# Kernel optimization log

Measured on AMD Instinct MI355X. Metric: run time of the kernel, lower is better.

Reference implementation:

```python
import jax, jax.numpy as jnp
import numpy as np

B, S, D, H = 4, 2048, 512, 8  # batch, seq, input_dim=feature_dim, n_heads


def setup_inputs() -> dict:
    key = jax.random.key(0)
    ks = jax.random.split(key, 12)
    s = 1.0 / np.sqrt(D)
    return {
        "q": jax.random.normal(ks[0], (B, S, D), jnp.float32),
        "k": jax.random.normal(ks[1], (B, S, D), jnp.float32),
        "v": jax.random.normal(ks[2], (B, S, D), jnp.float32),
        "mask": jax.random.randint(ks[3], (B, S), 0, 2, jnp.int32),
        "wq": jax.random.uniform(ks[4], (D, D), jnp.float32, -s, s),
        "bq": jax.random.uniform(ks[5], (D,), jnp.float32, -s, s),
        "wk": jax.random.uniform(ks[6], (D, D), jnp.float32, -s, s),
        "bk": jax.random.uniform(ks[7], (D,), jnp.float32, -s, s),
        "wv": jax.random.uniform(ks[8], (D, D), jnp.float32, -s, s),
        "bv": jax.random.uniform(ks[9], (D,), jnp.float32, -s, s),
        "wd": jax.random.uniform(ks[10], (D, D), jnp.float32, -s, s),
        "bd": jax.random.uniform(ks[11], (D,), jnp.float32, -s, s),
    }


def reference(q, k, v, mask, wq, bq, wk, bk, wv, bv, wd, bd):
    hd = D // H
    # linear projections [B,S,D]
    qp = q @ wq + bq
    kp = k @ wk + bk
    vp = v @ wv + bv
    # split heads -> [B,H,S,hd]
    split = lambda x: x.reshape(B, S, H, hd).transpose(0, 2, 1, 3)
    qh, kh, vh = split(qp), split(kp), split(vp)
    # scaled dot-product attention with additive mask [B,1,1,S]
    scores = jnp.einsum("bhqd,bhkd->bhqk", qh, kh) / np.sqrt(hd)
    scores = scores + mask.astype(scores.dtype)[:, None, None, :] * (-1e9)
    weights = jax.nn.softmax(scores, axis=-1)
    attn = jnp.einsum("bhqk,bhkd->bhqd", weights, vh)
    # merge heads -> [B,S,D], final dense
    attn = attn.transpose(0, 2, 1, 3).reshape(B, S, D)
    return attn @ wd + bd
```

## Files before the change

kernel.cpp:

```cpp
#include <hip/hip_runtime.h>
#include <hip/hip_bf16.h>
#include <cmath>

typedef __bf16 bf16;
typedef __attribute__((ext_vector_type(8))) __bf16 bf16x8;
typedef __attribute__((ext_vector_type(4))) __bf16 bf16x4;
typedef __attribute__((ext_vector_type(4))) float f32x4;
typedef __attribute__((ext_vector_type(16))) float f32x16;

#define LOG2E 1.4426950408889634f

__global__ __launch_bounds__(256)
void prep_w(const float* __restrict__ w0, const float* __restrict__ w1,
            const float* __restrict__ w2, const float* __restrict__ w3,
            bf16* __restrict__ wt)
{
    const float* W = (blockIdx.z == 0) ? w0 : (blockIdx.z == 1) ? w1
                   : (blockIdx.z == 2) ? w2 : w3;
    bf16* WT = wt + (size_t)blockIdx.z * 512 * 512;

    __shared__ bf16 t[64][72];
    const int k0 = blockIdx.x * 64, n0 = blockIdx.y * 64;
    const int tid = threadIdx.x;
    {
        const int row = tid >> 2;
        const int c0 = (tid & 3) * 16;
        const float* src = W + (size_t)(k0 + row) * 512 + n0 + c0;
#pragma unroll
        for (int i = 0; i < 16; i += 4) {
            f32x4 f = *(const f32x4*)(src + i);
            t[c0 + i + 0][row] = (bf16)f[0];
            t[c0 + i + 1][row] = (bf16)f[1];
            t[c0 + i + 2][row] = (bf16)f[2];
            t[c0 + i + 3][row] = (bf16)f[3];
        }
    }
    __syncthreads();
    {
        const int nrow = tid >> 2;
        const int c0 = (tid & 3) * 16;
        bf16* dst = WT + (size_t)(n0 + nrow) * 512 + k0 + c0;
        *(bf16x8*)(dst)     = *(const bf16x8*)&t[nrow][c0];
        *(bf16x8*)(dst + 8) = *(const bf16x8*)&t[nrow][c0 + 8];
    }
}

__global__ __launch_bounds__(256)
void proj_kernel(const float* __restrict__ qin, const float* __restrict__ kin,
                 const float* __restrict__ vin, const bf16* __restrict__ wt,
                 const float* __restrict__ bq, const float* __restrict__ bk,
                 const float* __restrict__ bv, bf16* __restrict__ qp,
                 bf16* __restrict__ kp, bf16* __restrict__ vpT)
{
    const int z = blockIdx.z;
    const float* A    = (z == 0) ? qin : (z == 1) ? kin : vin;
    const bf16* WT    = wt + (size_t)z * 262144;
    const float* bias = (z == 0) ? bq : (z == 1) ? bk : bv;
    const float scale = (z == 0) ? 0.125f * LOG2E : 1.0f;

    const int row0 = blockIdx.x * 64;
    const int col0 = blockIdx.y * 128;
    const int tid = threadIdx.x;
    const int wave = tid >> 6, lane = tid & 63;
    const int wr = wave >> 1, wc = wave & 1;
    const int g = lane >> 4, r = lane & 15;

    __shared__ bf16 As[64][72];
    __shared__ bf16 Bs[128][72];

    const int arow = tid >> 2, ak0 = (tid & 3) * 16;
    const int brow = tid >> 1, bk0 = (tid & 1) * 32;

    f32x4 a0, a1, a2, a3;
    bf16x8 b0, b1, b2, b3;
    {
        const float* asrc = A + (size_t)(row0 + arow) * 512 + ak0;
        a0 = *(const f32x4*)(asrc);     a1 = *(const f32x4*)(asrc + 4);
        a2 = *(const f32x4*)(asrc + 8); a3 = *(const f32x4*)(asrc + 12);
        const bf16* bsrc = WT + (size_t)(col0 + brow) * 512 + bk0;
        b0 = *(const bf16x8*)(bsrc);      b1 = *(const bf16x8*)(bsrc + 8);
        b2 = *(const bf16x8*)(bsrc + 16); b3 = *(const bf16x8*)(bsrc + 24);
    }

    f32x4 acc[2][4] = {};

    for (int kt = 0; kt < 512; kt += 64) {
        {
            bf16x8 v0, v1;
#pragma unroll
            for (int i = 0; i < 4; i++) {
                v0[i] = (bf16)a0[i]; v0[4+i] = (bf16)a1[i];
                v1[i] = (bf16)a2[i]; v1[4+i] = (bf16)a3[i];
            }
            *(bf16x8*)&As[arow][ak0]     = v0;
            *(bf16x8*)&As[arow][ak0 + 8] = v1;
            *(bf16x8*)&Bs[brow][bk0]      = b0;
            *(bf16x8*)&Bs[brow][bk0 +  8] = b1;
            *(bf16x8*)&Bs[brow][bk0 + 16] = b2;
            *(bf16x8*)&Bs[brow][bk0 + 24] = b3;
        }
        __syncthreads();

        if (kt + 64 < 512) {
            const float* asrc = A + (size_t)(row0 + arow) * 512 + kt + 64 + ak0;
            a0 = *(const f32x4*)(asrc);     a1 = *(const f32x4*)(asrc + 4);
            a2 = *(const f32x4*)(asrc + 8); a3 = *(const f32x4*)(asrc + 12);
            const bf16* bsrc = WT + (size_t)(col0 + brow) * 512 + kt + 64 + bk0;
            b0 = *(const bf16x8*)(bsrc);      b1 = *(const bf16x8*)(bsrc + 8);
            b2 = *(const bf16x8*)(bsrc + 16); b3 = *(const bf16x8*)(bsrc + 24);
        }

#pragma unroll
        for (int kk = 0; kk < 64; kk += 32) {
            bf16x8 af[2], bfr[4];
#pragma unroll
            for (int mf = 0; mf < 2; mf++)
                af[mf] = *(const bf16x8*)&As[wr*32 + mf*16 + r][kk + g*8];
#pragma unroll
            for (int nf = 0; nf < 4; nf++)
                bfr[nf] = *(const bf16x8*)&Bs[wc*64 + nf*16 + r][kk + g*8];
#pragma unroll
            for (int mf = 0; mf < 2; mf++)
#pragma unroll
                for (int nf = 0; nf < 4; nf++)
                    acc[mf][nf] = __builtin_amdgcn_mfma_f32_16x16x32_bf16(
                        af[mf], bfr[nf], acc[mf][nf], 0, 0, 0);
        }
        __syncthreads();
    }

#pragma unroll
    for (int mf = 0; mf < 2; mf++) {
#pragma unroll
        for (int nf = 0; nf < 4; nf++) {
            const int rbase = row0 + wr*32 + mf*16 + g*4;
            const int ccol  = col0 + wc*64 + nf*16 + r;
            const float bi = bias[ccol];
            const int h = ccol >> 6, hd = ccol & 63;
            if (z < 2) {
                bf16* C = (z == 0) ? qp : kp;
#pragma unroll
                for (int j = 0; j < 4; j++) {
                    const int rrow = rbase + j;
                    const int b = rrow >> 11, s = rrow & 2047;
                    C[(((size_t)(b*8 + h) * 2048) + s) * 64 + hd] =
                        (bf16)((acc[mf][nf][j] + bi) * scale);
                }
            } else {
                const int b = rbase >> 11, s = rbase & 2047;
                bf16x4 pk;
#pragma unroll
                for (int j = 0; j < 4; j++) pk[j] = (bf16)(acc[mf][nf][j] + bi);
                *(bf16x4*)(vpT + ((size_t)(b*8 + h) * 64 + hd) * 2048 + s) = pk;
            }
        }
    }
}

__global__ __launch_bounds__(256)
void dense_kernel(const bf16* __restrict__ ab, const bf16* __restrict__ WT,
                  const float* __restrict__ bias, float* __restrict__ out)
{
    const int row0 = blockIdx.x * 64;
    const int col0 = blockIdx.y * 128;
    const int tid = threadIdx.x;
    const int wave = tid >> 6, lane = tid & 63;
    const int wr = wave >> 1, wc = wave & 1;
    const int g = lane >> 4, r = lane & 15;

    __shared__ bf16 As[64][72];
    __shared__ bf16 Bs[128][72];

    const int arow = tid >> 2, ak0 = (tid & 3) * 16;
    const int brow = tid >> 1, bk0 = (tid & 1) * 32;

    bf16x8 aR0, aR1, b0, b1, b2, b3;
    {
        const bf16* asrc = ab + (size_t)(row0 + arow) * 512 + ak0;
        aR0 = *(const bf16x8*)(asrc); aR1 = *(const bf16x8*)(asrc + 8);
        const bf16* bsrc = WT + (size_t)(col0 + brow) * 512 + bk0;
        b0 = *(const bf16x8*)(bsrc);      b1 = *(const bf16x8*)(bsrc + 8);
        b2 = *(const bf16x8*)(bsrc + 16); b3 = *(const bf16x8*)(bsrc + 24);
    }

    f32x4 acc[2][4] = {};

    for (int kt = 0; kt < 512; kt += 64) {
        *(bf16x8*)&As[arow][ak0]     = aR0;
        *(bf16x8*)&As[arow][ak0 + 8] = aR1;
        *(bf16x8*)&Bs[brow][bk0]      = b0;
        *(bf16x8*)&Bs[brow][bk0 +  8] = b1;
        *(bf16x8*)&Bs[brow][bk0 + 16] = b2;
        *(bf16x8*)&Bs[brow][bk0 + 24] = b3;
        __syncthreads();

        if (kt + 64 < 512) {
            const bf16* asrc = ab + (size_t)(row0 + arow) * 512 + kt + 64 + ak0;
            aR0 = *(const bf16x8*)(asrc); aR1 = *(const bf16x8*)(asrc + 8);
            const bf16* bsrc = WT + (size_t)(col0 + brow) * 512 + kt + 64 + bk0;
            b0 = *(const bf16x8*)(bsrc);      b1 = *(const bf16x8*)(bsrc + 8);
            b2 = *(const bf16x8*)(bsrc + 16); b3 = *(const bf16x8*)(bsrc + 24);
        }

#pragma unroll
        for (int kk = 0; kk < 64; kk += 32) {
            bf16x8 af[2], bfr[4];
#pragma unroll
            for (int mf = 0; mf < 2; mf++)
                af[mf] = *(const bf16x8*)&As[wr*32 + mf*16 + r][kk + g*8];
#pragma unroll
            for (int nf = 0; nf < 4; nf++)
                bfr[nf] = *(const bf16x8*)&Bs[wc*64 + nf*16 + r][kk + g*8];
#pragma unroll
            for (int mf = 0; mf < 2; mf++)
#pragma unroll
                for (int nf = 0; nf < 4; nf++)
                    acc[mf][nf] = __builtin_amdgcn_mfma_f32_16x16x32_bf16(
                        af[mf], bfr[nf], acc[mf][nf], 0, 0, 0);
        }
        __syncthreads();
    }

#pragma unroll
    for (int mf = 0; mf < 2; mf++) {
#pragma unroll
        for (int nf = 0; nf < 4; nf++) {
            const int rbase = row0 + wr*32 + mf*16 + g*4;
            const int ccol  = col0 + wc*64 + nf*16 + r;
            const float bi = bias[ccol];
#pragma unroll
            for (int j = 0; j < 4; j++)
                out[(size_t)(rbase + j) * 512 + ccol] = acc[mf][nf][j] + bi;
        }
    }
}

__global__ __launch_bounds__(256)
void attn_kernel(const bf16* __restrict__ qp, const bf16* __restrict__ kp,
                 const bf16* __restrict__ vpT, const int* __restrict__ mask,
                 bf16* __restrict__ attn)
{
    const int bh = blockIdx.x;
    const int qt = blockIdx.y;
    const int b = bh >> 3, h = bh & 7;
    const int tid = threadIdx.x;
    const int w = tid >> 6, lane = tid & 63;
    const int c = lane & 31;
    const int hi = lane >> 5;

    __shared__ bf16 Ks[2][64][72];
    __shared__ bf16 Vt[2][64][72];
    __shared__ __align__(16) float madd2[2048];

    const size_t head_base = (size_t)(b*8 + h) * 2048 * 64;
    const int q0 = qt * 128;
    const bf16* kbase = kp  + head_base;
    const bf16* vbase = vpT + head_base;

    {
        const int4* m4 = (const int4*)(mask + b * 2048);
#pragma unroll
        for (int i = 0; i < 2; i++) {
            const int4 mv = m4[tid*2 + i];
            f32x4 f;
            f[0] = mv.x ? -1.4426950e9f : 0.f;
            f[1] = mv.y ? -1.4426950e9f : 0.f;
            f[2] = mv.z ? -1.4426950e9f : 0.f;
            f[3] = mv.w ? -1.4426950e9f : 0.f;
            *(f32x4*)&madd2[tid*8 + i*4] = f;
        }
    }

    bf16x8 qf[4];
    {
        const bf16* qsrc = qp + head_base + (size_t)(q0 + w*32 + c) * 64 + hi*8;
#pragma unroll
        for (int kstep = 0; kstep < 4; kstep++)
            qf[kstep] = *(const bf16x8*)(qsrc + kstep*16);
    }

    const int srow = tid >> 2;
    const int sc0  = (tid & 3) * 16;
    bf16x8 kr0, kr1, vr0, vr1;
    kr0 = *(const bf16x8*)(kbase + (size_t)srow * 64 + sc0);
    kr1 = *(const bf16x8*)(kbase + (size_t)srow * 64 + sc0 + 8);
    vr0 = *(const bf16x8*)(vbase + (size_t)srow * 2048 + sc0);
    vr1 = *(const bf16x8*)(vbase + (size_t)srow * 2048 + sc0 + 8);
    *(bf16x8*)&Ks[0][srow][sc0]     = kr0;
    *(bf16x8*)&Ks[0][srow][sc0 + 8] = kr1;
    *(bf16x8*)&Vt[0][srow][sc0]     = vr0;
    *(bf16x8*)&Vt[0][srow][sc0 + 8] = vr1;

    float m_run = -INFINITY, l_run = 0.f;
    f32x16 oT0 = {}, oT1 = {};

    int it = 0;
    for (int kt = 0; kt < 2048; kt += 64, it ^= 1) {
        __syncthreads();
        const bool more = (kt + 64) < 2048;
        if (more) {
            kr0 = *(const bf16x8*)(kbase + (size_t)(kt+64+srow)*64 + sc0);
            kr1 = *(const bf16x8*)(kbase + (size_t)(kt+64+srow)*64 + sc0 + 8);
            vr0 = *(const bf16x8*)(vbase + (size_t)srow*2048 + kt+64 + sc0);
            vr1 = *(const bf16x8*)(vbase + (size_t)srow*2048 + kt+64 + sc0 + 8);
        }

        f32x16 sa0 = {}, sa1 = {};
        __builtin_amdgcn_s_setprio(1);
#pragma unroll
        for (int kstep = 0; kstep < 4; kstep++) {
            const bf16x8 k0 = *(const bf16x8*)&Ks[it][c][kstep*16 + hi*8];
            const bf16x8 k1 = *(const bf16x8*)&Ks[it][32 + c][kstep*16 + hi*8];
            sa0 = __builtin_amdgcn_mfma_f32_32x32x16_bf16(k0, qf[kstep], sa0, 0, 0, 0);
            sa1 = __builtin_amdgcn_mfma_f32_32x32x16_bf16(k1, qf[kstep], sa1, 0, 0, 0);
        }
        __builtin_amdgcn_s_setprio(0);

        float mx = -INFINITY;
#pragma unroll
        for (int t = 0; t < 4; t++) {
            const f32x4 ma0 = *(const f32x4*)&madd2[kt +      t*8 + hi*4];
            const f32x4 ma1 = *(const f32x4*)&madd2[kt + 32 + t*8 + hi*4];
#pragma unroll
            for (int j = 0; j < 4; j++) {
                sa0[t*4+j] += ma0[j];
                sa1[t*4+j] += ma1[j];
                mx = fmaxf(mx, fmaxf(sa0[t*4+j], sa1[t*4+j]));
            }
        }
        if (!__all(mx <= m_run + 11.54f)) {
            mx = fmaxf(mx, __shfl_xor(mx, 32, 64));
            const float mn = fmaxf(m_run, mx);
            const float corr = __builtin_amdgcn_exp2f(m_run - mn);
            oT0 *= corr; oT1 *= corr; l_run *= corr;
            m_run = mn;
        }

        float psum = 0.f;
        unsigned int z[2][4][2];
#pragma unroll
        for (int t = 0; t < 4; t++) {
            float p0 = __builtin_amdgcn_exp2f(sa0[t*4+0] - m_run);
            float p1 = __builtin_amdgcn_exp2f(sa0[t*4+1] - m_run);
            float p2 = __builtin_amdgcn_exp2f(sa0[t*4+2] - m_run);
            float p3 = __builtin_amdgcn_exp2f(sa0[t*4+3] - m_run);
            asm("v_cvt_pk_bf16_f32 %0, %1, %2" : "=v"(z[0][t][0]) : "v"(p0), "v"(p1));
            asm("v_cvt_pk_bf16_f32 %0, %1, %2" : "=v"(z[0][t][1]) : "v"(p2), "v"(p3));
            psum += (p0 + p1) + (p2 + p3);
            float q4 = __builtin_amdgcn_exp2f(sa1[t*4+0] - m_run);
            float q5 = __builtin_amdgcn_exp2f(sa1[t*4+1] - m_run);
            float q6 = __builtin_amdgcn_exp2f(sa1[t*4+2] - m_run);
            float q7 = __builtin_amdgcn_exp2f(sa1[t*4+3] - m_run);
            asm("v_cvt_pk_bf16_f32 %0, %1, %2" : "=v"(z[1][t][0]) : "v"(q4), "v"(q5));
            asm("v_cvt_pk_bf16_f32 %0, %1, %2" : "=v"(z[1][t][1]) : "v"(q6), "v"(q7));
            psum += (q4 + q5) + (q6 + q7);
        }
        psum += __shfl_xor(psum, 32, 64);
        l_run += psum;

        __builtin_amdgcn_s_setprio(1);
#pragma unroll
        for (int kg = 0; kg < 2; kg++) {
#pragma unroll
            for (int ksl = 0; ksl < 2; ksl++) {
                unsigned int a0 = z[kg][2*ksl][0], a1 = z[kg][2*ksl][1];
                unsigned int b0 = z[kg][2*ksl+1][0], b1 = z[kg][2*ksl+1][1];
                asm volatile("v_permlane32_swap_b32 %0, %1" : "+v"(a0), "+v"(b0));
                asm volatile("v_permlane32_swap_b32 %0, %1" : "+v"(a1), "+v"(b1));
                union { unsigned int u[4]; bf16x8 v; } pf;
                pf.u[0] = a0; pf.u[1] = a1; pf.u[2] = b0; pf.u[3] = b1;
                const int kcol = (kg*2 + ksl)*16 + hi*8;
                const bf16x8 v0 = *(const bf16x8*)&Vt[it][c][kcol];
                const bf16x8 v1 = *(const bf16x8*)&Vt[it][32 + c][kcol];
                oT0 = __builtin_amdgcn_mfma_f32_32x32x16_bf16(v0, pf.v, oT0, 0, 0, 0);
                oT1 = __builtin_amdgcn_mfma_f32_32x32x16_bf16(v1, pf.v, oT1, 0, 0, 0);
            }
        }
        __builtin_amdgcn_s_setprio(0);

        if (more) {
            *(bf16x8*)&Ks[it^1][srow][sc0]     = kr0;
            *(bf16x8*)&Ks[it^1][srow][sc0 + 8] = kr1;
            *(bf16x8*)&Vt[it^1][srow][sc0]     = vr0;
            *(bf16x8*)&Vt[it^1][srow][sc0 + 8] = vr1;
        }
    }

    const float inv = 1.0f / l_run;
    const int s = q0 + w*32 + c;
    bf16* dst = attn + ((size_t)(b*2048) + s) * 512 + h*64;
#pragma unroll
    for (int t = 0; t < 4; t++) {
        bf16x4 o0, o1;
#pragma unroll
        for (int j = 0; j < 4; j++) {
            o0[j] = (bf16)(oT0[t*4+j] * inv);
            o1[j] = (bf16)(oT1[t*4+j] * inv);
        }
        *(bf16x4*)(dst +      t*8 + hi*4) = o0;
        *(bf16x4*)(dst + 32 + t*8 + hi*4) = o1;
    }
}

extern "C" void kernel_launch(void* const* d_in, const int* in_sizes, int n_in,
                              void* d_out, int out_size, void* d_ws, size_t ws_size,
                              hipStream_t stream)
{
    const float* q    = (const float*)d_in[0];
    const float* k    = (const float*)d_in[1];
    const float* v    = (const float*)d_in[2];
    const int*   mask = (const int*)  d_in[3];
    const float* wq   = (const float*)d_in[4];
    const float* bq   = (const float*)d_in[5];
    const float* wk   = (const float*)d_in[6];
    const float* bk   = (const float*)d_in[7];
    const float* wv   = (const float*)d_in[8];
    const float* bv   = (const float*)d_in[9];
    const float* wd   = (const float*)d_in[10];
    const float* bd   = (const float*)d_in[11];
    float* out = (float*)d_out;

    const size_t NELEM = (size_t)4 * 2048 * 512;
    bf16* qp  = (bf16*)d_ws;
    bf16* kp  = qp + NELEM;
    bf16* vpT = kp + NELEM;
    bf16* ab  = vpT + NELEM;
    bf16* wt  = ab + NELEM;

    prep_w<<<dim3(8, 8, 4), dim3(256), 0, stream>>>(wq, wk, wv, wd, wt);

    proj_kernel<<<dim3(128, 4, 3), dim3(256), 0, stream>>>(
        q, k, v, wt, bq, bk, bv, qp, kp, vpT);

    attn_kernel<<<dim3(32, 16), dim3(256), 0, stream>>>(qp, kp, vpT, mask, ab);

    dense_kernel<<<dim3(128, 4), dim3(256), 0, stream>>>(
        ab, wt + 3*262144, bd, out);
}
```

Before: 105.8 us.

## Split attention over the key dimension and merge partials in a combine kernel

Templates the attention kernel on a key-split factor and launches it with two key halves per query tile, doubling the block count. Each half writes unnormalised fp32 partial outputs plus its running max and sum, and a new combine kernel rescales and merges them into the bf16 attention buffer. The per-tile softmax is also reordered: the row max is taken from raw scores before the mask is added, and the mask add is folded into the exp2 argument with vectorised partial sums. This aims to raise occupancy and parallelism across the GPU's compute units, at the cost of extra fp32 partial-result traffic and one more kernel launch. It falls back to the unsplit path if the workspace is too small.

Result: slower. 121.7 us (+15.0%).

```diff
diff --git a/kernel.cpp b/kernel.cpp
--- a/kernel.cpp
+++ b/kernel.cpp
@@ -235,13 +235,17 @@
     }
 }
 
+template<int KSPLIT>
 __global__ __launch_bounds__(256)
 void attn_kernel(const bf16* __restrict__ qp, const bf16* __restrict__ kp,
                  const bf16* __restrict__ vpT, const int* __restrict__ mask,
-                 bf16* __restrict__ attn)
-{
+                 bf16* __restrict__ attn, float* __restrict__ pO,
+                 float* __restrict__ mArr, float* __restrict__ lArr)
+{
+    constexpr int NK = 2048 / KSPLIT;
     const int bh = blockIdx.x;
     const int qt = blockIdx.y;
+    const int sp = blockIdx.z;
     const int b = bh >> 3, h = bh & 7;
     const int tid = threadIdx.x;
     const int w = tid >> 6, lane = tid & 63;
@@ -250,24 +254,24 @@
 
     __shared__ bf16 Ks[2][64][72];
     __shared__ bf16 Vt[2][64][72];
-    __shared__ __align__(16) float madd2[2048];
+    __shared__ __align__(16) float madd2[NK];
 
     const size_t head_base = (size_t)(b*8 + h) * 2048 * 64;
     const int q0 = qt * 128;
+    const int kt0 = sp * NK;
     const bf16* kbase = kp  + head_base;
     const bf16* vbase = vpT + head_base;
 
     {
-        const int4* m4 = (const int4*)(mask + b * 2048);
-#pragma unroll
-        for (int i = 0; i < 2; i++) {
-            const int4 mv = m4[tid*2 + i];
+        const int4* m4 = (const int4*)(mask + b * 2048 + kt0);
+        for (int i = tid; i < NK/4; i += 256) {
+            const int4 mv = m4[i];
             f32x4 f;
             f[0] = mv.x ? -1.4426950e9f : 0.f;
             f[1] = mv.y ? -1.4426950e9f : 0.f;
             f[2] = mv.z ? -1.4426950e9f : 0.f;
             f[3] = mv.w ? -1.4426950e9f : 0.f;
-            *(f32x4*)&madd2[tid*8 + i*4] = f;
+            *(f32x4*)&madd2[i*4] = f;
         }
     }
 
@@ -282,10 +286,10 @@
     const int srow = tid >> 2;
     const int sc0  = (tid & 3) * 16;
     bf16x8 kr0, kr1, vr0, vr1;
-    kr0 = *(const bf16x8*)(kbase + (size_t)srow * 64 + sc0);
-    kr1 = *(const bf16x8*)(kbase + (size_t)srow * 64 + sc0 + 8);
-    vr0 = *(const bf16x8*)(vbase + (size_t)srow * 2048 + sc0);
-    vr1 = *(const bf16x8*)(vbase + (size_t)srow * 2048 + sc0 + 8);
+    kr0 = *(const bf16x8*)(kbase + (size_t)(kt0 + srow) * 64 + sc0);
+    kr1 = *(const bf16x8*)(kbase + (size_t)(kt0 + srow) * 64 + sc0 + 8);
+    vr0 = *(const bf16x8*)(vbase + (size_t)srow * 2048 + kt0 + sc0);
+    vr1 = *(const bf16x8*)(vbase + (size_t)srow * 2048 + kt0 + sc0 + 8);
     *(bf16x8*)&Ks[0][srow][sc0]     = kr0;
     *(bf16x8*)&Ks[0][srow][sc0 + 8] = kr1;
     *(bf16x8*)&Vt[0][srow][sc0]     = vr0;
@@ -295,14 +299,15 @@
     f32x16 oT0 = {}, oT1 = {};
 
     int it = 0;
-    for (int kt = 0; kt < 2048; kt += 64, it ^= 1) {
+    for (int kt = 0; kt < NK; kt += 64, it ^= 1) {
         __syncthreads();
-        const bool more = (kt + 64) < 2048;
+        const bool more = (kt + 64) < NK;
         if (more) {
-            kr0 = *(const bf16x8*)(kbase + (size_t)(kt+64+srow)*64 + sc0);
-            kr1 = *(const bf16x8*)(kbase + (size_t)(kt+64+srow)*64 + sc0 + 8);
-            vr0 = *(const bf16x8*)(vbase + (size_t)srow*2048 + kt+64 + sc0);
-            vr1 = *(const bf16x8*)(vbase + (size_t)srow*2048 + kt+64 + sc0 + 8);
+            const int kg = kt0 + kt + 64;
+            kr0 = *(const bf16x8*)(kbase + (size_t)(kg + srow)*64 + sc0);
+            kr1 = *(const bf16x8*)(kbase + (size_t)(kg + srow)*64 + sc0 + 8);
+            vr0 = *(const bf16x8*)(vbase + (size_t)srow*2048 + kg + sc0);
+            vr1 = *(const bf16x8*)(vbase + (size_t)srow*2048 + kg + sc0 + 8);
         }
 
         f32x16 sa0 = {}, sa1 = {};
@@ -316,45 +321,42 @@
         }
         __builtin_amdgcn_s_setprio(0);
 
-        float mx = -INFINITY;
+        f32x4 vm;
+#pragma unroll
+        for (int j = 0; j < 4; j++)
+            vm[j] = fmaxf(fmaxf(fmaxf(sa0[j], sa0[4+j]),
+                                fmaxf(sa0[8+j], sa0[12+j])),
+                          fmaxf(fmaxf(sa1[j], sa1[4+j]),
+                                fmaxf(sa1[8+j], sa1[12+j])));
+        const float mx = fmaxf(fmaxf(vm[0], vm[1]), fmaxf(vm[2], vm[3]));
+
+        if (!__all(mx <= m_run + 11.54f)) {
+            float mr = fmaxf(mx, __shfl_xor(mx, 32, 64));
+            const float mn = fmaxf(m_run, mr);
+            const float corr = __builtin_amdgcn_exp2f(m_run - mn);
+            oT0 *= corr; oT1 *= corr; l_run *= corr;
+            m_run = mn;
+        }
+
+        f32x4 ps4 = {0.f, 0.f, 0.f, 0.f};
+        unsigned int z[2][4][2];
 #pragma unroll
         for (int t = 0; t < 4; t++) {
             const f32x4 ma0 = *(const f32x4*)&madd2[kt +      t*8 + hi*4];
             const f32x4 ma1 = *(const f32x4*)&madd2[kt + 32 + t*8 + hi*4];
+            f32x4 e0, e1;
 #pragma unroll
             for (int j = 0; j < 4; j++) {
-                sa0[t*4+j] += ma0[j];
-                sa1[t*4+j] += ma1[j];
-                mx = fmaxf(mx, fmaxf(sa0[t*4+j], sa1[t*4+j]));
+                e0[j] = __builtin_amdgcn_exp2f(sa0[t*4+j] + ma0[j] - m_run);
+                e1[j] = __builtin_amdgcn_exp2f(sa1[t*4+j] + ma1[j] - m_run);
             }
-        }
-        if (!__all(mx <= m_run + 11.54f)) {
-            mx = fmaxf(mx, __shfl_xor(mx, 32, 64));
-            const float mn = fmaxf(m_run, mx);
-            const float corr = __builtin_amdgcn_exp2f(m_run - mn);
-            oT0 *= corr; oT1 *= corr; l_run *= corr;
-            m_run = mn;
-        }
-
-        float psum = 0.f;
-        unsigned int z[2][4][2];
-#pragma unroll
-        for (int t = 0; t < 4; t++) {
-            float p0 = __builtin_amdgcn_exp2f(sa0[t*4+0] - m_run);
-            float p1 = __builtin_amdgcn_exp2f(sa0[t*4+1] - m_run);
-            float p2 = __builtin_amdgcn_exp2f(sa0[t*4+2] - m_run);
-            float p3 = __builtin_amdgcn_exp2f(sa0[t*4+3] - m_run);
-            asm("v_cvt_pk_bf16_f32 %0, %1, %2" : "=v"(z[0][t][0]) : "v"(p0), "v"(p1));
-            asm("v_cvt_pk_bf16_f32 %0, %1, %2" : "=v"(z[0][t][1]) : "v"(p2), "v"(p3));
-            psum += (p0 + p1) + (p2 + p3);
-            float q4 = __builtin_amdgcn_exp2f(sa1[t*4+0] - m_run);
-            float q5 = __builtin_amdgcn_exp2f(sa1[t*4+1] - m_run);
-            float q6 = __builtin_amdgcn_exp2f(sa1[t*4+2] - m_run);
-            float q7 = __builtin_amdgcn_exp2f(sa1[t*4+3] - m_run);
-            asm("v_cvt_pk_bf16_f32 %0, %1, %2" : "=v"(z[1][t][0]) : "v"(q4), "v"(q5));
-            asm("v_cvt_pk_bf16_f32 %0, %1, %2" : "=v"(z[1][t][1]) : "v"(q6), "v"(q7));
-            psum += (q4 + q5) + (q6 + q7);
-        }
+            asm("v_cvt_pk_bf16_f32 %0, %1, %2" : "=v"(z[0][t][0]) : "v"(e0[0]), "v"(e0[1]));
+            asm("v_cvt_pk_bf16_f32 %0, %1, %2" : "=v"(z[0][t][1]) : "v"(e0[2]), "v"(e0[3]));
+            asm("v_cvt_pk_bf16_f32 %0, %1, %2" : "=v"(z[1][t][0]) : "v"(e1[0]), "v"(e1[1]));
+            asm("v_cvt_pk_bf16_f32 %0, %1, %2" : "=v"(z[1][t][1]) : "v"(e1[2]), "v"(e1[3]));
+            ps4 += e0 + e1;
+        }
+        float psum = (ps4[0] + ps4[1]) + (ps4[2] + ps4[3]);
         psum += __shfl_xor(psum, 32, 64);
         l_run += psum;
 
@@ -386,20 +388,67 @@
         }
     }
 
-    const float inv = 1.0f / l_run;
-    const int s = q0 + w*32 + c;
-    bf16* dst = attn + ((size_t)(b*2048) + s) * 512 + h*64;
-#pragma unroll
-    for (int t = 0; t < 4; t++) {
-        bf16x4 o0, o1;
-#pragma unroll
-        for (int j = 0; j < 4; j++) {
-            o0[j] = (bf16)(oT0[t*4+j] * inv);
-            o1[j] = (bf16)(oT1[t*4+j] * inv);
-        }
-        *(bf16x4*)(dst +      t*8 + hi*4) = o0;
-        *(bf16x4*)(dst + 32 + t*8 + hi*4) = o1;
-    }
+    if constexpr (KSPLIT == 1) {
+        const float inv = 1.0f / l_run;
+        const int s = q0 + w*32 + c;
+        bf16* dst = attn + ((size_t)(b*2048) + s) * 512 + h*64;
+#pragma unroll
+        for (int t = 0; t < 4; t++) {
+            bf16x4 o0, o1;
+#pragma unroll
+            for (int j = 0; j < 4; j++) {
+                o0[j] = (bf16)(oT0[t*4+j] * inv);
+                o1[j] = (bf16)(oT1[t*4+j] * inv);
+            }
+            *(bf16x4*)(dst +      t*8 + hi*4) = o0;
+            *(bf16x4*)(dst + 32 + t*8 + hi*4) = o1;
+        }
+    } else {
+        const int q = q0 + w*32 + c;
+        const size_t gq = (size_t)sp * 65536 + (size_t)bh * 2048 + q;
+        float* po = pO + gq * 64;
+#pragma unroll
+        for (int t = 0; t < 4; t++) {
+            f32x4 x0, x1;
+#pragma unroll
+            for (int j = 0; j < 4; j++) { x0[j] = oT0[t*4+j]; x1[j] = oT1[t*4+j]; }
+            *(f32x4*)(po +      t*8 + hi*4) = x0;
+            *(f32x4*)(po + 32 + t*8 + hi*4) = x1;
+        }
+        if (hi == 0) { mArr[gq] = m_run; lArr[gq] = l_run; }
+    }
+}
+
+__global__ __launch_bounds__(256)
+void combine_kernel(const float* __restrict__ pO, const float* __restrict__ mArr,
+                    const float* __restrict__ lArr, bf16* __restrict__ attn)
+{
+    const int gid = blockIdx.x * 256 + threadIdx.x;
+    const int g = gid >> 3;
+    const int d0 = (gid & 7) * 8;
+
+    const float m1 = mArr[g],        m2 = mArr[65536 + g];
+    const float l1 = lArr[g],        l2 = lArr[65536 + g];
+    const float m  = fmaxf(m1, m2);
+    const float w1 = __builtin_amdgcn_exp2f(m1 - m);
+    const float w2 = __builtin_amdgcn_exp2f(m2 - m);
+    const float inv = 1.0f / (w1 * l1 + w2 * l2);
+    const float a1 = w1 * inv, a2 = w2 * inv;
+
+    const float* p1 = pO + (size_t)g * 64 + d0;
+    const float* p2 = p1 + (size_t)65536 * 64;
+    const f32x4 x0 = *(const f32x4*)(p1), x1 = *(const f32x4*)(p1 + 4);
+    const f32x4 y0 = *(const f32x4*)(p2), y1 = *(const f32x4*)(p2 + 4);
+
+    bf16x8 o;
+#pragma unroll
+    for (int j = 0; j < 4; j++) {
+        o[j]     = (bf16)(x0[j] * a1 + y0[j] * a2);
+        o[4 + j] = (bf16)(x1[j] * a1 + y1[j] * a2);
+    }
+    const int bh = g >> 11, q = g & 2047;
+    const int b = bh >> 3, h = bh & 7;
+    *(bf16x8*)(attn + ((size_t)(b*2048 + q)) * 512 + h*64 + d0) = o;
 }
 
 extern "C" void kernel_launch(void* const* d_in, const int* in_sizes, int n_in,
@@ -426,13 +475,24 @@
     bf16* vpT = kp + NELEM;
     bf16* ab  = vpT + NELEM;
     bf16* wt  = ab + NELEM;
+    float* pO = (float*)(wt + 4 * 262144);
+    float* mA = pO + (size_t)2 * 65536 * 64;
+    float* lA = mA + (size_t)2 * 65536;
+    const size_t need = (size_t)((char*)(lA + (size_t)2 * 65536) - (char*)d_ws);
 
     prep_w<<<dim3(8, 8, 4), dim3(256), 0, stream>>>(wq, wk, wv, wd, wt);
 
     proj_kernel<<<dim3(128, 4, 3), dim3(256), 0, stream>>>(
         q, k, v, wt, bq, bk, bv, qp, kp, vpT);
 
-    attn_kernel<<<dim3(32, 16), dim3(256), 0, stream>>>(qp, kp, vpT, mask, ab);
+    if (ws_size >= need) {
+        attn_kernel<2><<<dim3(32, 16, 2), dim3(256), 0, stream>>>(
+            qp, kp, vpT, mask, ab, pO, mA, lA);
+        combine_kernel<<<dim3(2048), dim3(256), 0, stream>>>(pO, mA, lA, ab);
+    } else {
+        attn_kernel<1><<<dim3(32, 16, 1), dim3(256), 0, stream>>>(
+            qp, kp, vpT, mask, ab, pO, mA, lA);
+    }
 
     dense_kernel<<<dim3(128, 4), dim3(256), 0, stream>>>(
         ab, wt + 3*262144, bd, out);
```

## Enlarge projection tiles and move softmax row sums onto MFMA

Applied to the files above, without the earlier changes.

The projection GEMM tile grows from 64x128 to 128x128 rows per block, halving the grid and reusing each weight tile over twice as many rows. In attention, the mask bias now initialises the score accumulators instead of being added afterwards, and the row max uses a tree reduction. The per-thread exp sums and cross-lane shuffle are replaced by an extra MFMA against a ones vector that accumulates the row sums. This trades VALU additions for matrix-core work, at the cost of more registers in both kernels and bf16-rounded probabilities in the denominator.

After: 112.4 us. 6.2% more time.

```diff
diff --git a/kernel.cpp b/kernel.cpp
--- a/kernel.cpp
+++ b/kernel.cpp
@@ -58,69 +58,68 @@
     const float* bias = (z == 0) ? bq : (z == 1) ? bk : bv;
     const float scale = (z == 0) ? 0.125f * LOG2E : 1.0f;
 
-    const int row0 = blockIdx.x * 64;
+    const int row0 = blockIdx.x * 128;
     const int col0 = blockIdx.y * 128;
     const int tid = threadIdx.x;
     const int wave = tid >> 6, lane = tid & 63;
     const int wr = wave >> 1, wc = wave & 1;
     const int g = lane >> 4, r = lane & 15;
 
-    __shared__ bf16 As[64][72];
+    __shared__ bf16 As[128][72];
     __shared__ bf16 Bs[128][72];
 
-    const int arow = tid >> 2, ak0 = (tid & 3) * 16;
+    const int arow = tid >> 1, ak0 = (tid & 1) * 32;
     const int brow = tid >> 1, bk0 = (tid & 1) * 32;
 
-    f32x4 a0, a1, a2, a3;
-    bf16x8 b0, b1, b2, b3;
+    f32x4 a[8];
+    bf16x8 bwr[4];
     {
         const float* asrc = A + (size_t)(row0 + arow) * 512 + ak0;
-        a0 = *(const f32x4*)(asrc);     a1 = *(const f32x4*)(asrc + 4);
-        a2 = *(const f32x4*)(asrc + 8); a3 = *(const f32x4*)(asrc + 12);
+#pragma unroll
+        for (int i = 0; i < 8; i++) a[i] = *(const f32x4*)(asrc + i*4);
         const bf16* bsrc = WT + (size_t)(col0 + brow) * 512 + bk0;
-        b0 = *(const bf16x8*)(bsrc);      b1 = *(const bf16x8*)(bsrc + 8);
-        b2 = *(const bf16x8*)(bsrc + 16); b3 = *(const bf16x8*)(bsrc + 24);
-    }
-
-    f32x4 acc[2][4] = {};
+#pragma unroll
+        for (int i = 0; i < 4; i++) bwr[i] = *(const bf16x8*)(bsrc + i*8);
+    }
+
+    f32x4 acc[4][4] = {};
 
     for (int kt = 0; kt < 512; kt += 64) {
         {
-            bf16x8 v0, v1;
 #pragma unroll
             for (int i = 0; i < 4; i++) {
-                v0[i] = (bf16)a0[i]; v0[4+i] = (bf16)a1[i];
-                v1[i] = (bf16)a2[i]; v1[4+i] = (bf16)a3[i];
+                bf16x8 v;
+#pragma unroll
+                for (int j = 0; j < 4; j++) {
+                    v[j]   = (bf16)a[2*i][j];
+                    v[4+j] = (bf16)a[2*i+1][j];
+                }
+                *(bf16x8*)&As[arow][ak0 + i*8] = v;
+                *(bf16x8*)&Bs[brow][bk0 + i*8] = bwr[i];
             }
-            *(bf16x8*)&As[arow][ak0]     = v0;
-            *(bf16x8*)&As[arow][ak0 + 8] = v1;
-            *(bf16x8*)&Bs[brow][bk0]      = b0;
-            *(bf16x8*)&Bs[brow][bk0 +  8] = b1;
-            *(bf16x8*)&Bs[brow][bk0 + 16] = b2;
-            *(bf16x8*)&Bs[brow][bk0 + 24] = b3;
         }
         __syncthreads();
 
         if (kt + 64 < 512) {
             const float* asrc = A + (size_t)(row0 + arow) * 512 + kt + 64 + ak0;
-            a0 = *(const f32x4*)(asrc);     a1 = *(const f32x4*)(asrc + 4);
-            a2 = *(const f32x4*)(asrc + 8); a3 = *(const f32x4*)(asrc + 12);
+#pragma unroll
+            for (int i = 0; i < 8; i++) a[i] = *(const f32x4*)(asrc + i*4);
             const bf16* bsrc = WT + (size_t)(col0 + brow) * 512 + kt + 64 + bk0;
-            b0 = *(const bf16x8*)(bsrc);      b1 = *(const bf16x8*)(bsrc + 8);
-            b2 = *(const bf16x8*)(bsrc + 16); b3 = *(const bf16x8*)(bsrc + 24);
+#pragma unroll
+            for (int i = 0; i < 4; i++) bwr[i] = *(const bf16x8*)(bsrc + i*8);
         }
 
 #pragma unroll
         for (int kk = 0; kk < 64; kk += 32) {
-            bf16x8 af[2], bfr[4];
-#pragma unroll
-            for (int mf = 0; mf < 2; mf++)
-                af[mf] = *(const bf16x8*)&As[wr*32 + mf*16 + r][kk + g*8];
+            bf16x8 af[4], bfr[4];
+#pragma unroll
+            for (int mf = 0; mf < 4; mf++)
+                af[mf] = *(const bf16x8*)&As[wr*64 + mf*16 + r][kk + g*8];
 #pragma unroll
             for (int nf = 0; nf < 4; nf++)
                 bfr[nf] = *(const bf16x8*)&Bs[wc*64 + nf*16 + r][kk + g*8];
 #pragma unroll
-            for (int mf = 0; mf < 2; mf++)
+            for (int mf = 0; mf < 4; mf++)
 #pragma unroll
                 for (int nf = 0; nf < 4; nf++)
                     acc[mf][nf] = __builtin_amdgcn_mfma_f32_16x16x32_bf16(
@@ -130,10 +129,10 @@
     }
 
 #pragma unroll
-    for (int mf = 0; mf < 2; mf++) {
+    for (int mf = 0; mf < 4; mf++) {
 #pragma unroll
         for (int nf = 0; nf < 4; nf++) {
-            const int rbase = row0 + wr*32 + mf*16 + g*4;
+            const int rbase = row0 + wr*64 + mf*16 + g*4;
             const int ccol  = col0 + wc*64 + nf*16 + r;
             const float bi = bias[ccol];
             const int h = ccol >> 6, hd = ccol & 63;
@@ -291,8 +290,14 @@
     *(bf16x8*)&Vt[0][srow][sc0]     = vr0;
     *(bf16x8*)&Vt[0][srow][sc0 + 8] = vr1;
 
-    float m_run = -INFINITY, l_run = 0.f;
+    float m_run = -INFINITY;
     f32x16 oT0 = {}, oT1 = {};
+    f32x16 lac = {};
+    bf16x8 ones;
+#pragma unroll
+    for (int i = 0; i < 8; i++) ones[i] = (bf16)1.0f;
+
+    union f16x4q { f32x16 v; f32x4 q[4]; };
 
     int it = 0;
     for (int kt = 0; kt < 2048; kt += 64, it ^= 1) {
@@ -305,58 +310,56 @@
             vr1 = *(const bf16x8*)(vbase + (size_t)srow*2048 + kt+64 + sc0 + 8);
         }
 
-        f32x16 sa0 = {}, sa1 = {};
+        f16x4q sa0, sa1;
+#pragma unroll
+        for (int t = 0; t < 4; t++) {
+            sa0.q[t] = *(const f32x4*)&madd2[kt +      t*8 + hi*4];
+            sa1.q[t] = *(const f32x4*)&madd2[kt + 32 + t*8 + hi*4];
+        }
+
         __builtin_amdgcn_s_setprio(1);
 #pragma unroll
         for (int kstep = 0; kstep < 4; kstep++) {
             const bf16x8 k0 = *(const bf16x8*)&Ks[it][c][kstep*16 + hi*8];
             const bf16x8 k1 = *(const bf16x8*)&Ks[it][32 + c][kstep*16 + hi*8];
-            sa0 = __builtin_amdgcn_mfma_f32_32x32x16_bf16(k0, qf[kstep], sa0, 0, 0, 0);
-            sa1 = __builtin_amdgcn_mfma_f32_32x32x16_bf16(k1, qf[kstep], sa1, 0, 0, 0);
+            sa0.v = __builtin_amdgcn_mfma_f32_32x32x16_bf16(k0, qf[kstep], sa0.v, 0, 0, 0);
+            sa1.v = __builtin_amdgcn_mfma_f32_32x32x16_bf16(k1, qf[kstep], sa1.v, 0, 0, 0);
         }
         __builtin_amdgcn_s_setprio(0);
 
-        float mx = -INFINITY;
+        f32x4 vm;
+#pragma unroll
+        for (int j = 0; j < 4; j++)
+            vm[j] = fmaxf(fmaxf(fmaxf(sa0.v[j], sa0.v[4+j]),
+                                fmaxf(sa0.v[8+j], sa0.v[12+j])),
+                          fmaxf(fmaxf(sa1.v[j], sa1.v[4+j]),
+                                fmaxf(sa1.v[8+j], sa1.v[12+j])));
+        const float mx = fmaxf(fmaxf(vm[0], vm[1]), fmaxf(vm[2], vm[3]));
+
+        if (!__all(mx <= m_run + 11.54f)) {
+            float mr = fmaxf(mx, __shfl_xor(mx, 32, 64));
+            const float mn = fmaxf(m_run, mr);
+            const float corr = __builtin_amdgcn_exp2f(m_run - mn);
+            oT0 *= corr; oT1 *= corr; lac *= corr;
+            m_run = mn;
+        }
+
+        unsigned int z[2][4][2];
 #pragma unroll
         for (int t = 0; t < 4; t++) {
-            const f32x4 ma0 = *(const f32x4*)&madd2[kt +      t*8 + hi*4];
-            const f32x4 ma1 = *(const f32x4*)&madd2[kt + 32 + t*8 + hi*4];
-#pragma unroll
-            for (int j = 0; j < 4; j++) {
-                sa0[t*4+j] += ma0[j];
-                sa1[t*4+j] += ma1[j];
-                mx = fmaxf(mx, fmaxf(sa0[t*4+j], sa1[t*4+j]));
-            }
-        }
-        if (!__all(mx <= m_run + 11.54f)) {
-            mx = fmaxf(mx, __shfl_xor(mx, 32, 64));
-            const float mn = fmaxf(m_run, mx);
-            const float corr = __builtin_amdgcn_exp2f(m_run - mn);
-            oT0 *= corr; oT1 *= corr; l_run *= corr;
-            m_run = mn;
-        }
-
-        float psum = 0.f;
-        unsigned int z[2][4][2];
-#pragma unroll
-        for (int t = 0; t < 4; t++) {
-            float p0 = __builtin_amdgcn_exp2f(sa0[t*4+0] - m_run);
-            float p1 = __builtin_amdgcn_exp2f(sa0[t*4+1] - m_run);
-            float p2 = __builtin_amdgcn_exp2f(sa0[t*4+2] - m_run);
-            float p3 = __builtin_amdgcn_exp2f(sa0[t*4+3] - m_run);
-            asm("v_cvt_pk_bf16_f32 %0, %1, %2" : "=v"(z[0][t][0]) : "v"(p0), "v"(p1));
-            asm("v_cvt_pk_bf16_f32 %0, %1, %2" : "=v"(z[0][t][1]) : "v"(p2), "v"(p3));
-            psum += (p0 + p1) + (p2 + p3);
-            float q4 = __builtin_amdgcn_exp2f(sa1[t*4+0] - m_run);
-            float q5 = __builtin_amdgcn_exp2f(sa1[t*4+1] - m_run);
-            float q6 = __builtin_amdgcn_exp2f(sa1[t*4+2] - m_run);
-            float q7 = __builtin_amdgcn_exp2f(sa1[t*4+3] - m_run);
-            asm("v_cvt_pk_bf16_f32 %0, %1, %2" : "=v"(z[1][t][0]) : "v"(q4), "v"(q5));
-            asm("v_cvt_pk_bf16_f32 %0, %1, %2" : "=v"(z[1][t][1]) : "v"(q6), "v"(q7));
-            psum += (q4 + q5) + (q6 + q7);
-        }
-        psum += __shfl_xor(psum, 32, 64);
-        l_run += psum;
+            float e0 = __builtin_amdgcn_exp2f(sa0.v[t*4+0] - m_run);
+            float e1 = __builtin_amdgcn_exp2f(sa0.v[t*4+1] - m_run);
+            float e2 = __builtin_amdgcn_exp2f(sa0.v[t*4+2] - m_run);
+            float e3 = __builtin_amdgcn_exp2f(sa0.v[t*4+3] - m_run);
+            asm("v_cvt_pk_bf16_f32 %0, %1, %2" : "=v"(z[0][t][0]) : "v"(e0), "v"(e1));
+            asm("v_cvt_pk_bf16_f32 %0, %1, %2" : "=v"(z[0][t][1]) : "v"(e2), "v"(e3));
+            float f0 = __builtin_amdgcn_exp2f(sa1.v[t*4+0] - m_run);
+            float f1 = __builtin_amdgcn_exp2f(sa1.v[t*4+1] - m_run);
+            float f2 = __builtin_amdgcn_exp2f(sa1.v[t*4+2] - m_run);
+            float f3 = __builtin_amdgcn_exp2f(sa1.v[t*4+3] - m_run);
+            asm("v_cvt_pk_bf16_f32 %0, %1, %2" : "=v"(z[1][t][0]) : "v"(f0), "v"(f1));
+            asm("v_cvt_pk_bf16_f32 %0, %1, %2" : "=v"(z[1][t][1]) : "v"(f2), "v"(f3));
+        }
 
         __builtin_amdgcn_s_setprio(1);
 #pragma unroll
@@ -374,6 +377,7 @@
                 const bf16x8 v1 = *(const bf16x8*)&Vt[it][32 + c][kcol];
                 oT0 = __builtin_amdgcn_mfma_f32_32x32x16_bf16(v0, pf.v, oT0, 0, 0, 0);
                 oT1 = __builtin_amdgcn_mfma_f32_32x32x16_bf16(v1, pf.v, oT1, 0, 0, 0);
+                lac = __builtin_amdgcn_mfma_f32_32x32x16_bf16(ones, pf.v, lac, 0, 0, 0);
             }
         }
         __builtin_amdgcn_s_setprio(0);
@@ -386,7 +390,7 @@
         }
     }
 
-    const float inv = 1.0f / l_run;
+    const float inv = 1.0f / lac[0];
     const int s = q0 + w*32 + c;
     bf16* dst = attn + ((size_t)(b*2048) + s) * 512 + h*64;
 #pragma unroll
@@ -429,7 +433,7 @@
 
     prep_w<<<dim3(8, 8, 4), dim3(256), 0, stream>>>(wq, wk, wv, wd, wt);
 
-    proj_kernel<<<dim3(128, 4, 3), dim3(256), 0, stream>>>(
+    proj_kernel<<<dim3(64, 4, 3), dim3(256), 0, stream>>>(
         q, k, v, wt, bq, bk, bv, qp, kp, vpT);
 
     attn_kernel<<<dim3(32, 16), dim3(256), 0, stream>>>(qp, kp, vpT, mask, ab);
```

## Drop LDS staging in attention; read K/V directly from global memory

Applied to the files above, without the earlier changes.

The attention kernel no longer stages K and V tiles through double-buffered shared memory with __syncthreads. Each wave now loads its MFMA operands straight from global memory, relying on L2/cache reuse across the four waves. The additive mask is precomputed into a float buffer by a new small kernel and preloaded as the score accumulator init, and blocks are remapped with a swizzle so that the heads sharing an XCD get consecutive query tiles. This removes barriers and LDS traffic, but each wave now issues redundant global loads and memory latency is exposed inside the loop without an explicit prefetch.

New measurement: 190.1 us. 79.7% more time.

```diff
diff --git a/kernel.cpp b/kernel.cpp
--- a/kernel.cpp
+++ b/kernel.cpp
@@ -9,6 +9,13 @@
 typedef __attribute__((ext_vector_type(16))) float f32x16;
 
 #define LOG2E 1.4426950408889634f
+
+__global__ __launch_bounds__(256)
+void mask_kernel(const int* __restrict__ mask, float* __restrict__ madd)
+{
+    const int gid = blockIdx.x * 256 + threadIdx.x;
+    madd[gid] = mask[gid] ? -1.4426950e9f : 0.f;
+}
 
 __global__ __launch_bounds__(256)
 void prep_w(const float* __restrict__ w0, const float* __restrict__ w1,
@@ -237,39 +244,26 @@
 
 __global__ __launch_bounds__(256)
 void attn_kernel(const bf16* __restrict__ qp, const bf16* __restrict__ kp,
-                 const bf16* __restrict__ vpT, const int* __restrict__ mask,
+                 const bf16* __restrict__ vpT, const float* __restrict__ madd,
                  bf16* __restrict__ attn)
 {
-    const int bh = blockIdx.x;
-    const int qt = blockIdx.y;
+    const int i = blockIdx.x;
+    const int swz = (i & 7) * 64 + (i >> 3);
+    const int bh = swz >> 4;
+    const int qt = swz & 15;
     const int b = bh >> 3, h = bh & 7;
     const int tid = threadIdx.x;
     const int w = tid >> 6, lane = tid & 63;
     const int c = lane & 31;
     const int hi = lane >> 5;
 
-    __shared__ bf16 Ks[2][64][72];
-    __shared__ bf16 Vt[2][64][72];
-    __shared__ __align__(16) float madd2[2048];
-
     const size_t head_base = (size_t)(b*8 + h) * 2048 * 64;
     const int q0 = qt * 128;
-    const bf16* kbase = kp  + head_base;
-    const bf16* vbase = vpT + head_base;
-
-    {
-        const int4* m4 = (const int4*)(mask + b * 2048);
-#pragma unroll
-        for (int i = 0; i < 2; i++) {
-            const int4 mv = m4[tid*2 + i];
-            f32x4 f;
-            f[0] = mv.x ? -1.4426950e9f : 0.f;
-            f[1] = mv.y ? -1.4426950e9f : 0.f;
-            f[2] = mv.z ? -1.4426950e9f : 0.f;
-            f[3] = mv.w ? -1.4426950e9f : 0.f;
-            *(f32x4*)&madd2[tid*8 + i*4] = f;
-        }
-    }
+    const bf16* krow0 = kp  + head_base + (size_t)c * 64;
+    const bf16* krow1 = krow0 + 32 * 64;
+    const bf16* vrow0 = vpT + head_base + (size_t)c * 2048;
+    const bf16* vrow1 = vrow0 + 32 * 2048;
+    const float* mrow = madd + b * 2048;
 
     bf16x8 qf[4];
     {
@@ -279,82 +273,63 @@
             qf[kstep] = *(const bf16x8*)(qsrc + kstep*16);
     }
 
-    const int srow = tid >> 2;
-    const int sc0  = (tid & 3) * 16;
-    bf16x8 kr0, kr1, vr0, vr1;
-    kr0 = *(const bf16x8*)(kbase + (size_t)srow * 64 + sc0);
-    kr1 = *(const bf16x8*)(kbase + (size_t)srow * 64 + sc0 + 8);
-    vr0 = *(const bf16x8*)(vbase + (size_t)srow * 2048 + sc0);
-    vr1 = *(const bf16x8*)(vbase + (size_t)srow * 2048 + sc0 + 8);
-    *(bf16x8*)&Ks[0][srow][sc0]     = kr0;
-    *(bf16x8*)&Ks[0][srow][sc0 + 8] = kr1;
-    *(bf16x8*)&Vt[0][srow][sc0]     = vr0;
-    *(bf16x8*)&Vt[0][srow][sc0 + 8] = vr1;
-
     float m_run = -INFINITY, l_run = 0.f;
     f32x16 oT0 = {}, oT1 = {};
 
-    int it = 0;
-    for (int kt = 0; kt < 2048; kt += 64, it ^= 1) {
-        __syncthreads();
-        const bool more = (kt + 64) < 2048;
-        if (more) {
-            kr0 = *(const bf16x8*)(kbase + (size_t)(kt+64+srow)*64 + sc0);
-            kr1 = *(const bf16x8*)(kbase + (size_t)(kt+64+srow)*64 + sc0 + 8);
-            vr0 = *(const bf16x8*)(vbase + (size_t)srow*2048 + kt+64 + sc0);
-            vr1 = *(const bf16x8*)(vbase + (size_t)srow*2048 + kt+64 + sc0 + 8);
-        }
-
-        f32x16 sa0 = {}, sa1 = {};
+    union f16x4q { f32x16 v; f32x4 q[4]; };
+
+    for (int kt = 0; kt < 2048; kt += 64) {
+        f16x4q sa0, sa1;
+#pragma unroll
+        for (int t = 0; t < 4; t++) {
+            sa0.q[t] = *(const f32x4*)&mrow[kt +      t*8 + hi*4];
+            sa1.q[t] = *(const f32x4*)&mrow[kt + 32 + t*8 + hi*4];
+        }
+
         __builtin_amdgcn_s_setprio(1);
 #pragma unroll
         for (int kstep = 0; kstep < 4; kstep++) {
-            const bf16x8 k0 = *(const bf16x8*)&Ks[it][c][kstep*16 + hi*8];
-            const bf16x8 k1 = *(const bf16x8*)&Ks[it][32 + c][kstep*16 + hi*8];
-            sa0 = __builtin_amdgcn_mfma_f32_32x32x16_bf16(k0, qf[kstep], sa0, 0, 0, 0);
-            sa1 = __builtin_amdgcn_mfma_f32_32x32x16_bf16(k1, qf[kstep], sa1, 0, 0, 0);
+            const bf16x8 k0 = *(const bf16x8*)(krow0 + (size_t)kt*64 + kstep*16 + hi*8);
+            const bf16x8 k1 = *(const bf16x8*)(krow1 + (size_t)kt*64 + kstep*16 + hi*8);
+            sa0.v = __builtin_amdgcn_mfma_f32_32x32x16_bf16(k0, qf[kstep], sa0.v, 0, 0, 0);
+            sa1.v = __builtin_amdgcn_mfma_f32_32x32x16_bf16(k1, qf[kstep], sa1.v, 0, 0, 0);
         }
         __builtin_amdgcn_s_setprio(0);
 
-        float mx = -INFINITY;
-#pragma unroll
-        for (int t = 0; t < 4; t++) {
-            const f32x4 ma0 = *(const f32x4*)&madd2[kt +      t*8 + hi*4];
-            const f32x4 ma1 = *(const f32x4*)&madd2[kt + 32 + t*8 + hi*4];
-#pragma unroll
-            for (int j = 0; j < 4; j++) {
-                sa0[t*4+j] += ma0[j];
-                sa1[t*4+j] += ma1[j];
-                mx = fmaxf(mx, fmaxf(sa0[t*4+j], sa1[t*4+j]));
-            }
-        }
+        f32x4 vm;
+#pragma unroll
+        for (int j = 0; j < 4; j++)
+            vm[j] = fmaxf(fmaxf(fmaxf(sa0.v[j], sa0.v[4+j]),
+                                fmaxf(sa0.v[8+j], sa0.v[12+j])),
+                          fmaxf(fmaxf(sa1.v[j], sa1.v[4+j]),
+                                fmaxf(sa1.v[8+j], sa1.v[12+j])));
+        const float mx = fmaxf(fmaxf(vm[0], vm[1]), fmaxf(vm[2], vm[3]));
+
         if (!__all(mx <= m_run + 11.54f)) {
-            mx = fmaxf(mx, __shfl_xor(mx, 32, 64));
-            const float mn = fmaxf(m_run, mx);
+            float mr = fmaxf(mx, __shfl_xor(mx, 32, 64));
+            const float mn = fmaxf(m_run, mr);
             const float corr = __builtin_amdgcn_exp2f(m_run - mn);
             oT0 *= corr; oT1 *= corr; l_run *= corr;
             m_run = mn;
         }
 
-        float psum = 0.f;
+        f32x4 ps4 = {0.f, 0.f, 0.f, 0.f};
         unsigned int z[2][4][2];
 #pragma unroll
         for (int t = 0; t < 4; t++) {
-            float p0 = __builtin_amdgcn_exp2f(sa0[t*4+0] - m_run);
-            float p1 = __builtin_amdgcn_exp2f(sa0[t*4+1] - m_run);
-            float p2 = __builtin_amdgcn_exp2f(sa0[t*4+2] - m_run);
-            float p3 = __builtin_amdgcn_exp2f(sa0[t*4+3] - m_run);
-            asm("v_cvt_pk_bf16_f32 %0, %1, %2" : "=v"(z[0][t][0]) : "v"(p0), "v"(p1));
-            asm("v_cvt_pk_bf16_f32 %0, %1, %2" : "=v"(z[0][t][1]) : "v"(p2), "v"(p3));
-            psum += (p0 + p1) + (p2 + p3);
-            float q4 = __builtin_amdgcn_exp2f(sa1[t*4+0] - m_run);
-            float q5 = __builtin_amdgcn_exp2f(sa1[t*4+1] - m_run);
-            float q6 = __builtin_amdgcn_exp2f(sa1[t*4+2] - m_run);
-            float q7 = __builtin_amdgcn_exp2f(sa1[t*4+3] - m_run);
-            asm("v_cvt_pk_bf16_f32 %0, %1, %2" : "=v"(z[1][t][0]) : "v"(q4), "v"(q5));
-            asm("v_cvt_pk_bf16_f32 %0, %1, %2" : "=v"(z[1][t][1]) : "v"(q6), "v"(q7));
-            psum += (q4 + q5) + (q6 + q7);
-        }
+            f32x4 e0, e1;
+#pragma unroll
+            for (int j = 0; j < 4; j++) {
+                e0[j] = __builtin_amdgcn_exp2f(sa0.v[t*4+j] - m_run);
+                e1[j] = __builtin_amdgcn_exp2f(sa1.v[t*4+j] - m_run);
+            }
+            asm("v_cvt_pk_bf16_f32 %0, %1, %2" : "=v"(z[0][t][0]) : "v"(e0[0]), "v"(e0[1]));
+            asm("v_cvt_pk_bf16_f32 %0, %1, %2" : "=v"(z[0][t][1]) : "v"(e0[2]), "v"(e0[3]));
+            asm("v_cvt_pk_bf16_f32 %0, %1, %2" : "=v"(z[1][t][0]) : "v"(e1[0]), "v"(e1[1]));
+            asm("v_cvt_pk_bf16_f32 %0, %1, %2" : "=v"(z[1][t][1]) : "v"(e1[2]), "v"(e1[3]));
+            ps4 += e0 + e1;
+        }
+        float psum = (ps4[0] + ps4[1]) + (ps4[2] + ps4[3]);
         psum += __shfl_xor(psum, 32, 64);
         l_run += psum;
 
@@ -369,21 +344,14 @@
                 asm volatile("v_permlane32_swap_b32 %0, %1" : "+v"(a1), "+v"(b1));
                 union { unsigned int u[4]; bf16x8 v; } pf;
                 pf.u[0] = a0; pf.u[1] = a1; pf.u[2] = b0; pf.u[3] = b1;
-                const int kcol = (kg*2 + ksl)*16 + hi*8;
-                const bf16x8 v0 = *(const bf16x8*)&Vt[it][c][kcol];
-                const bf16x8 v1 = *(const bf16x8*)&Vt[it][32 + c][kcol];
+                const int kcol = kt + (kg*2 + ksl)*16 + hi*8;
+                const bf16x8 v0 = *(const bf16x8*)(vrow0 + kcol);
+                const bf16x8 v1 = *(const bf16x8*)(vrow1 + kcol);
                 oT0 = __builtin_amdgcn_mfma_f32_32x32x16_bf16(v0, pf.v, oT0, 0, 0, 0);
                 oT1 = __builtin_amdgcn_mfma_f32_32x32x16_bf16(v1, pf.v, oT1, 0, 0, 0);
             }
         }
         __builtin_amdgcn_s_setprio(0);
-
-        if (more) {
-            *(bf16x8*)&Ks[it^1][srow][sc0]     = kr0;
-            *(bf16x8*)&Ks[it^1][srow][sc0 + 8] = kr1;
-            *(bf16x8*)&Vt[it^1][srow][sc0]     = vr0;
-            *(bf16x8*)&Vt[it^1][srow][sc0 + 8] = vr1;
-        }
     }
 
     const float inv = 1.0f / l_run;
@@ -426,13 +394,16 @@
     bf16* vpT = kp + NELEM;
     bf16* ab  = vpT + NELEM;
     bf16* wt  = ab + NELEM;
+    float* madd = (float*)(wt + 4 * 262144);
+
+    mask_kernel<<<dim3(32), dim3(256), 0, stream>>>(mask, madd);
 
     prep_w<<<dim3(8, 8, 4), dim3(256), 0, stream>>>(wq, wk, wv, wd, wt);
 
     proj_kernel<<<dim3(128, 4, 3), dim3(256), 0, stream>>>(
         q, k, v, wt, bq, bk, bv, qp, kp, vpT);
 
-    attn_kernel<<<dim3(32, 16), dim3(256), 0, stream>>>(qp, kp, vpT, mask, ab);
+    attn_kernel<<<dim3(512), dim3(256), 0, stream>>>(qp, kp, vpT, madd, ab);
 
     dense_kernel<<<dim3(128, 4), dim3(256), 0, stream>>>(
         ab, wt + 3*262144, bd, out);
```
